# Performance work log

Measured on AMD Instinct MI355X. Metric: run time of the kernel, lower is better.

Reference implementation:

```python
import jax, jax.numpy as jnp
import numpy as np

N_NODES = 100000
N_EDGES = 1600000
IN_DIM = 256
HEADS = 4
OUT_DIM = 32
NEG_SLOPE = 0.2


def setup_inputs() -> dict:
    key = jax.random.key(0)
    ks = jax.random.split(key, 6)
    x = jax.random.normal(ks[0], (N_NODES, IN_DIM), dtype=jnp.float32)
    # xavier-ish init scale for fc and attention vectors
    W = jax.random.normal(ks[1], (IN_DIM, HEADS * OUT_DIM), dtype=jnp.float32) * (1.0 / np.sqrt(IN_DIM))
    attn_l = jax.random.normal(ks[2], (HEADS, OUT_DIM), dtype=jnp.float32) * (1.0 / np.sqrt(OUT_DIM))
    attn_r = jax.random.normal(ks[3], (HEADS, OUT_DIM), dtype=jnp.float32) * (1.0 / np.sqrt(OUT_DIM))
    src = jax.random.randint(ks[4], (N_EDGES,), 0, N_NODES, dtype=jnp.int32)
    dst = jax.random.randint(ks[5], (N_EDGES,), 0, N_NODES, dtype=jnp.int32)
    return {"x": x, "W": W, "attn_l": attn_l, "attn_r": attn_r, "src": src, "dst": dst}


def reference(x, W, attn_l, attn_r, src, dst):
    N = x.shape[0]
    H, D = attn_l.shape
    # shared linear projection (feat_drop = 0)
    feat = (x @ W).reshape(N, H, D)                      # [N,H,D]
    el = jnp.sum(feat * attn_l, axis=-1)                 # [N,H]
    er = jnp.sum(feat * attn_r, axis=-1)                 # [N,H]
    e = jax.nn.leaky_relu(el[src] + er[dst], NEG_SLOPE)  # [E,H]
    # edge softmax over incoming edges of each destination node
    m = jax.ops.segment_max(e, dst, num_segments=N)      # [N,H]
    m = jnp.where(jnp.isfinite(m), m, 0.0)               # zero-in-degree guard
    ex = jnp.exp(e - m[dst])                             # [E,H]
    denom = jax.ops.segment_sum(ex, dst, num_segments=N) # [N,H]
    a = ex / jnp.maximum(denom[dst], 1e-9)               # [E,H] (attn_drop = 0)
    # weighted scatter-add aggregation
    out = jax.ops.segment_sum(a[:, :, None] * feat[src], dst, num_segments=N)  # [N,H,D]
    # head mean (the .mean(1) in GAT1.forward)
    return out.mean(axis=1)                              # [N,D]
```

## Files before the change

kernel.cpp:

```cpp
#include <hip/hip_runtime.h>
#include <math.h>

#define NN 100000
#define NE 1600000
#define IN_DIM 256
#define HD 128
#define NEG_SLOPE 0.2f

#define B1SH 9
#define NPB (1 << B1SH)
#define NB1 ((NN + NPB - 1) / NPB)
#define SC_BLOCKS ((NE / 4 + 1023) / 1024)
#define SCP 392
#define GEMM_BLOCKS ((NN + 63) / 64)
#define D2_GRID (SC_BLOCKS * 5)

typedef __attribute__((ext_vector_type(8))) __bf16 bf16x8;
typedef __attribute__((ext_vector_type(4))) float floatx4;
typedef __attribute__((ext_vector_type(2))) float f32x2;

__device__ inline unsigned short f2bf(float f) {
    unsigned int b = __float_as_uint(f);
    b += 0x7fffu + ((b >> 16) & 1u);
    return (unsigned short)(b >> 16);
}
__device__ inline unsigned int pk(float lo, float hi) {
    return (unsigned int)f2bf(lo) | ((unsigned int)f2bf(hi) << 16);
}
__device__ inline float lrelu(float v) { return (v > 0.f) ? v : v * NEG_SLOPE; }
__device__ inline f32x2 un2(unsigned int v) {
    f32x2 r;
    r.x = __uint_as_float(v << 16);
    r.y = __uint_as_float(v & 0xffff0000u);
    return r;
}

__global__ __launch_bounds__(256) void d1_kernel(const float* __restrict__ W,
                                                 unsigned int* __restrict__ wswz,
                                                 const int4* __restrict__ dst4,
                                                 int* __restrict__ gcnt2dT) {
    __shared__ int cnt[NB1];
    const int t = threadIdx.x;
    if (blockIdx.x < SC_BLOCKS) {
        for (int i = t; i < NB1; i += 256) cnt[i] = 0;
        __syncthreads();
        int base4 = blockIdx.x * 1024;
#pragma unroll
        for (int k = 0; k < 4; ++k) {
            int gi = base4 + k * 256 + t;
            if (gi < NE / 4) {
                int4 d = dst4[gi];
                atomicAdd(&cnt[d.x >> B1SH], 1);
                atomicAdd(&cnt[d.y >> B1SH], 1);
                atomicAdd(&cnt[d.z >> B1SH], 1);
                atomicAdd(&cnt[d.w >> B1SH], 1);
            }
        }
        __syncthreads();
        for (int i = t; i < NB1; i += 256)
            gcnt2dT[i * SCP + blockIdx.x] = cnt[i];
        if (blockIdx.x == 0)
            for (int i = t; i < NB1; i += 256)
                gcnt2dT[i * SCP + SC_BLOCKS] = 0;
    } else {
        int g = (blockIdx.x - SC_BLOCKS) * 256 + t;
        int lane = g & 63;
        int tt = (g >> 6) & 7;
        int c = g >> 9;
        int sub = lane & 15, quad = lane >> 4;
        int n = tt * 16 + sub;
        int kbase = c * 32 + quad * 8;
        unsigned int ob = (unsigned int)g * 4;
#pragma unroll
        for (int i = 0; i < 4; ++i) {
            float lo = W[(size_t)(kbase + 2 * i) * HD + n];
            float hi = W[(size_t)(kbase + 2 * i + 1) * HD + n];
            wswz[ob + i] = pk(lo, hi);
        }
    }
}

__global__ __launch_bounds__(256) void d2_kernel(const float* __restrict__ x,
                                                 const uint4* __restrict__ wswz,
                                                 const float* __restrict__ attn_l,
                                                 const float* __restrict__ attn_r,
                                                 unsigned short* __restrict__ featb,
                                                 float* __restrict__ el,
                                                 float* __restrict__ er,
                                                 const int4* __restrict__ src4,
                                                 const int4* __restrict__ dst4,
                                                 const int* __restrict__ gcnt2dT,
                                                 unsigned int* __restrict__ pkd,
                                                 int* __restrict__ regstart) {
    __shared__ int cnt[NB1];
    __shared__ int gbase[NB1];
    __shared__ int sh[256];
    const int t = threadIdx.x;
    const int bid = blockIdx.x;

    if (bid % 5 == 0) {
        const int b = bid / 5;
        int colsum = 0, mypre = 0;
        if (t < NB1) {
            const int4* rowp = (const int4*)(gcnt2dT + t * SCP);
#pragma unroll 7
            for (int q = 0; q < SCP / 4; ++q) {
                int4 v = rowp[q];
                int s4 = v.x + v.y + v.z + v.w;
                colsum += s4;
                int base = q * 4;
                if (base + 4 <= b) {
                    mypre += s4;
                } else {
                    if (base + 0 < b) mypre += v.x;
                    if (base + 1 < b) mypre += v.y;
                    if (base + 2 < b) mypre += v.z;
                    if (base + 3 < b) mypre += v.w;
                }
            }
        }
        sh[t] = (t < NB1) ? colsum : 0;
        __syncthreads();
        for (int o = 1; o < 256; o <<= 1) {
            int a = (t >= o) ? sh[t - o] : 0;
            __syncthreads();
            sh[t] += a;
            __syncthreads();
        }
        int rstart = sh[t] - ((t < NB1) ? colsum : 0);
        if (t < NB1) gbase[t] = rstart + mypre;
        if (b == 0 && t < NB1) regstart[t] = rstart;
        if (b == 0 && t == 0) regstart[NB1] = NE;
        for (int i = t; i < NB1; i += 256) cnt[i] = 0;
        __syncthreads();

        int base4 = b * 1024;
        unsigned int pkv[16];
        unsigned int brk[16];
#pragma unroll
        for (int k = 0; k < 4; ++k) {
            int gi = base4 + k * 256 + t;
            bool ok = gi < NE / 4;
            int gic = ok ? gi : 0;
            int4 s = src4[gic];
            int4 d = dst4[gic];
            int dd[4] = {d.x, d.y, d.z, d.w};
            int ss[4] = {s.x, s.y, s.z, s.w};
#pragma unroll
            for (int j4 = 0; j4 < 4; ++j4) {
                int e = k * 4 + j4;
                if (ok) {
                    int bk = dd[j4] >> B1SH;
                    int r = atomicAdd(&cnt[bk], 1);
                    brk[e] = ((unsigned int)bk << 12) | (unsigned int)r;
                    pkv[e] = ((unsigned int)(dd[j4] & (NPB - 1)) << 17) | (unsigned int)ss[j4];
                } else {
                    brk[e] = 0xFFFFFFFFu;
                }
            }
        }
        __syncthreads();
#pragma unroll
        for (int e = 0; e < 16; ++e) {
            if (brk[e] != 0xFFFFFFFFu) {
                int bk = brk[e] >> 12;
                int r = brk[e] & 0xFFF;
                pkd[gbase[bk] + r] = pkv[e];
            }
        }
    } else {
        const int gb = bid - 1 - bid / 5;
        if (gb >= GEMM_BLOCKS) return;
        const int lane = t & 63, wv = t >> 6;
        const int sub = lane & 15, quad = lane >> 4;
        const int row0 = gb * 64 + wv * 16;

        int m = row0 + sub;
        if (m >= NN) m = NN - 1;
        const float* xp = x + (size_t)m * IN_DIM + quad * 8;

        bf16x8 af[8];
#pragma unroll
        for (int h = 0; h < 2; ++h) {
            float4 raw[4][2];
#pragma unroll
            for (int c = 0; c < 4; ++c) {
                raw[c][0] = *(const float4*)(xp + (h * 4 + c) * 32);
                raw[c][1] = *(const float4*)(xp + (h * 4 + c) * 32 + 4);
            }
#pragma unroll
            for (int c = 0; c < 4; ++c) {
                uint4 au;
                au.x = pk(raw[c][0].x, raw[c][0].y);
                au.y = pk(raw[c][0].z, raw[c][0].w);
                au.z = pk(raw[c][1].x, raw[c][1].y);
                au.w = pk(raw[c][1].z, raw[c][1].w);
                af[h * 4 + c] = __builtin_bit_cast(bf16x8, au);
            }
        }

        floatx4 acc[8];
#pragma unroll
        for (int tt = 0; tt < 8; ++tt) acc[tt] = (floatx4){0.f, 0.f, 0.f, 0.f};

#pragma unroll
        for (int c = 0; c < 8; ++c) {
            uint4 bu[8];
#pragma unroll
            for (int tt = 0; tt < 8; ++tt) bu[tt] = wswz[(c * 8 + tt) * 64 + lane];
#pragma unroll
            for (int tt = 0; tt < 8; ++tt) {
                bf16x8 bfr = __builtin_bit_cast(bf16x8, bu[tt]);
                acc[tt] = __builtin_amdgcn_mfma_f32_16x16x32_bf16(af[c], bfr, acc[tt], 0, 0, 0);
            }
        }

        float al[8], ar[8];
#pragma unroll
        for (int tt = 0; tt < 8; ++tt) {
            al[tt] = attn_l[tt * 16 + sub];
            ar[tt] = attn_r[tt * 16 + sub];
        }

#pragma unroll
        for (int r = 0; r < 4; ++r) {
            int row = row0 + quad * 4 + r;
            uint4 fv;
            fv.x = pk(acc[0][r], acc[1][r]);
            fv.y = pk(acc[2][r], acc[3][r]);
            fv.z = pk(acc[4][r], acc[5][r]);
            fv.w = pk(acc[6][r], acc[7][r]);
            float pl[4], pr[4];
#pragma unroll
            for (int hh = 0; hh < 4; ++hh) {
                pl[hh] = acc[2 * hh][r] * al[2 * hh] + acc[2 * hh + 1][r] * al[2 * hh + 1];
                pr[hh] = acc[2 * hh][r] * ar[2 * hh] + acc[2 * hh + 1][r] * ar[2 * hh + 1];
            }
#pragma unroll
            for (int o = 1; o < 16; o <<= 1) {
#pragma unroll
                for (int hh = 0; hh < 4; ++hh) {
                    pl[hh] += __shfl_xor(pl[hh], o);
                    pr[hh] += __shfl_xor(pr[hh], o);
                }
            }
            if (row < NN) {
                *(uint4*)(featb + (size_t)row * HD + sub * 8) = fv;
                if (sub < 4) {
                    float vl = (sub == 0) ? pl[0] : (sub == 1) ? pl[1] : (sub == 2) ? pl[2] : pl[3];
                    float vr = (sub == 0) ? pr[0] : (sub == 1) ? pr[1] : (sub == 2) ? pr[2] : pr[3];
                    el[row * 4 + sub] = vl;
                    er[row * 4 + sub] = vr;
                }
            }
        }
    }
}

__global__ __launch_bounds__(1024) void build_kernel(const unsigned int* __restrict__ pkd,
                                                     const int* __restrict__ regstart,
                                                     int* __restrict__ offs,
                                                     int* __restrict__ csr_src) {
    __shared__ int fcnt[NPB];
    __shared__ int foffs[NPB];
    __shared__ int ssc[NPB];
    int b = blockIdx.x, t = threadIdx.x;
    int rs = regstart[b], re = regstart[b + 1];
    int n = re - rs;
    if (b == 0 && t == 0) offs[NN] = NE;

    if (t < NPB) fcnt[t] = 0;
    __syncthreads();
    for (int i = t; i < n; i += 1024) {
        unsigned int v = pkd[rs + i];
        atomicAdd(&fcnt[v >> 17], 1);
    }
    __syncthreads();
    int a = 0;
    if (t < NPB) { a = fcnt[t]; ssc[t] = a; }
    __syncthreads();
    for (int o = 1; o < NPB; o <<= 1) {
        int u = 0;
        if (t < NPB && t >= o) u = ssc[t - o];
        __syncthreads();
        if (t < NPB) ssc[t] += u;
        __syncthreads();
    }
    if (t < NPB) {
        foffs[t] = ssc[t] - a;
        int node = b * NPB + t;
        if (node < NN) offs[node] = rs + foffs[t];
        fcnt[t] = 0;
    }
    __syncthreads();
    int i = t;
    for (; i + 3072 < n; i += 4096) {
        unsigned int v0 = pkd[rs + i];
        unsigned int v1 = pkd[rs + i + 1024];
        unsigned int v2 = pkd[rs + i + 2048];
        unsigned int v3 = pkd[rs + i + 3072];
        int j0 = v0 >> 17, j1 = v1 >> 17, j2 = v2 >> 17, j3 = v3 >> 17;
        int r0 = atomicAdd(&fcnt[j0], 1);
        int r1 = atomicAdd(&fcnt[j1], 1);
        int r2 = atomicAdd(&fcnt[j2], 1);
        int r3 = atomicAdd(&fcnt[j3], 1);
        csr_src[rs + foffs[j0] + r0] = (int)(v0 & 0x1FFFFu);
        csr_src[rs + foffs[j1] + r1] = (int)(v1 & 0x1FFFFu);
        csr_src[rs + foffs[j2] + r2] = (int)(v2 & 0x1FFFFu);
        csr_src[rs + foffs[j3] + r3] = (int)(v3 & 0x1FFFFu);
    }
    for (; i < n; i += 1024) {
        unsigned int v = pkd[rs + i];
        int j = v >> 17;
        int r = atomicAdd(&fcnt[j], 1);
        csr_src[rs + foffs[j] + r] = (int)(v & 0x1FFFFu);
    }
}

#define CH 32
__global__ __launch_bounds__(256, 4) void aggregate_kernel(const uint4* __restrict__ featu4,
                                                           const float4* __restrict__ el4,
                                                           const float4* __restrict__ er4,
                                                           const int* __restrict__ offs,
                                                           const int* __restrict__ csr_src,
                                                           float* __restrict__ out) {
    __shared__ int    s_sv[4][4][CH + 1];
    __shared__ float4 s_a4[4][4][CH + 1];
    __shared__ int sdeg[16], smap[16];

    const int tid = threadIdx.x;
    const int lane = tid & 63, wv = tid >> 6;
    const int g = lane >> 4, sub = lane & 15;

    if (tid < 16) {
        int n0 = blockIdx.x * 16 + tid;
        sdeg[tid] = offs[n0 + 1] - offs[n0];
    }
    __syncthreads();
    if (tid < 16) {
        int d = sdeg[tid];
        int rank = 0;
#pragma unroll
        for (int j = 0; j < 16; ++j) {
            int dj = sdeg[j];
            rank += (dj < d) || (dj == d && j < tid);
        }
        smap[rank] = blockIdx.x * 16 + tid;
    }
    __syncthreads();
    const int node = smap[wv * 4 + g];
    const int beg = offs[node], end = offs[node + 1];

    const float4 erv = er4[node];
    float4 sm = make_float4(0.f, 0.f, 0.f, 0.f);
    f32x2 acc2[4];
#pragma unroll
    for (int i = 0; i < 4; ++i) acc2[i] = (f32x2){0.f, 0.f};

    for (int c0 = beg; c0 < end; c0 += CH) {
        int cnt = end - c0;
        if (cnt > CH) cnt = CH;

        int svr[2];
#pragma unroll
        for (int t = 0; t < 2; ++t) {
            int slot = sub + t * 16;
            int sv = (slot < cnt) ? csr_src[c0 + slot] : 0;
            svr[t] = sv;
            s_sv[wv][g][slot] = sv * 16;
        }

        uint4 ua[8], ub[8];
#pragma unroll
        for (int e = 0; e < 8; ++e)
            ua[e] = featu4[(size_t)s_sv[wv][g][e] + sub];

#pragma unroll
        for (int t = 0; t < 2; ++t) {
            int slot = sub + t * 16;
            float4 w = make_float4(0.f, 0.f, 0.f, 0.f);
            if (slot < cnt) {
                float4 e = el4[svr[t]];
                w.x = __expf(lrelu(e.x + erv.x));
                w.y = __expf(lrelu(e.y + erv.y));
                w.z = __expf(lrelu(e.z + erv.z));
                w.w = __expf(lrelu(e.w + erv.w));
                sm.x += w.x; sm.y += w.y; sm.z += w.z; sm.w += w.w;
            }
            s_a4[wv][g][slot] = w;
        }

        int rounds = (cnt + 7) >> 3;
        int jr = 0;
        while (true) {
            bool m1 = (jr + 1) < rounds;
            if (m1) {
                int nb = (jr + 1) << 3;
#pragma unroll
                for (int e = 0; e < 8; ++e)
                    ub[e] = featu4[(size_t)s_sv[wv][g][nb + e] + sub];
            }
            {
                int jb = jr << 3;
#pragma unroll
                for (int e = 0; e < 8; ++e) {
                    float4 we = s_a4[wv][g][jb + e];
                    uint4 u = ua[e];
                    f32x2 w0 = {we.x, we.x}, w1 = {we.y, we.y};
                    f32x2 w2 = {we.z, we.z}, w3 = {we.w, we.w};
                    acc2[0] = __builtin_elementwise_fma(w0, un2(u.x), acc2[0]);
                    acc2[1] = __builtin_elementwise_fma(w1, un2(u.y), acc2[1]);
                    acc2[2] = __builtin_elementwise_fma(w2, un2(u.z), acc2[2]);
                    acc2[3] = __builtin_elementwise_fma(w3, un2(u.w), acc2[3]);
                }
            }
            ++jr;
            if (!m1) break;
            bool m2 = (jr + 1) < rounds;
            if (m2) {
                int nb = (jr + 1) << 3;
#pragma unroll
                for (int e = 0; e < 8; ++e)
                    ua[e] = featu4[(size_t)s_sv[wv][g][nb + e] + sub];
            }
            {
                int jb = jr << 3;
#pragma unroll
                for (int e = 0; e < 8; ++e) {
                    float4 we = s_a4[wv][g][jb + e];
                    uint4 u = ub[e];
                    f32x2 w0 = {we.x, we.x}, w1 = {we.y, we.y};
                    f32x2 w2 = {we.z, we.z}, w3 = {we.w, we.w};
                    acc2[0] = __builtin_elementwise_fma(w0, un2(u.x), acc2[0]);
                    acc2[1] = __builtin_elementwise_fma(w1, un2(u.y), acc2[1]);
                    acc2[2] = __builtin_elementwise_fma(w2, un2(u.z), acc2[2]);
                    acc2[3] = __builtin_elementwise_fma(w3, un2(u.w), acc2[3]);
                }
            }
            ++jr;
            if (!m2) break;
        }
    }

#pragma unroll
    for (int o = 1; o < 16; o <<= 1) {
        sm.x += __shfl_xor(sm.x, o);
        sm.y += __shfl_xor(sm.y, o);
        sm.z += __shfl_xor(sm.z, o);
        sm.w += __shfl_xor(sm.w, o);
    }
    float ix = 1.f / fmaxf(sm.x, 1e-9f);
    float iy = 1.f / fmaxf(sm.y, 1e-9f);
    float iz = 1.f / fmaxf(sm.z, 1e-9f);
    float iw = 1.f / fmaxf(sm.w, 1e-9f);
    float ox = 0.25f * (acc2[0].x * ix + acc2[1].x * iy + acc2[2].x * iz + acc2[3].x * iw);
    float oy = 0.25f * (acc2[0].y * ix + acc2[1].y * iy + acc2[2].y * iz + acc2[3].y * iw);
    out[node * 32 + sub]      = ox;
    out[node * 32 + 16 + sub] = oy;
}

extern "C" void kernel_launch(void* const* d_in, const int* in_sizes, int n_in,
                              void* d_out, int out_size, void* d_ws, size_t ws_size,
                              hipStream_t stream) {
    const float* x      = (const float*)d_in[0];
    const float* W      = (const float*)d_in[1];
    const float* attn_l = (const float*)d_in[2];
    const float* attn_r = (const float*)d_in[3];
    const int*   src    = (const int*)d_in[4];
    const int*   dst    = (const int*)d_in[5];
    float* out = (float*)d_out;

    char* p = (char*)d_ws;
    auto alloc = [&](size_t bytes) -> void* {
        void* r = (void*)p;
        p += (bytes + 255) & ~(size_t)255;
        return r;
    };
    unsigned short* featb = (unsigned short*)alloc((size_t)NN * HD * 2);
    unsigned int*   wswz  = (unsigned int*)alloc(4096 * 16);
    float* el      = (float*)alloc((size_t)NN * 4 * 4);
    float* er      = (float*)alloc((size_t)NN * 4 * 4);
    int*   offs    = (int*)alloc((size_t)(NN + 1) * 4);
    unsigned int* pkd = (unsigned int*)alloc((size_t)NE * 4);
    int*   csr     = (int*)alloc((size_t)NE * 4);
    int*   gcnt2dT = (int*)alloc((size_t)NB1 * SCP * 4);
    int*   regstart= (int*)alloc((size_t)(NB1 + 1) * 4);

    d1_kernel<<<SC_BLOCKS + 16, 256, 0, stream>>>(W, wswz, (const int4*)dst, gcnt2dT);
    d2_kernel<<<D2_GRID, 256, 0, stream>>>(x, (const uint4*)wswz, attn_l, attn_r,
                                           featb, el, er,
                                           (const int4*)src, (const int4*)dst,
                                           gcnt2dT, pkd, regstart);
    build_kernel<<<NB1, 1024, 0, stream>>>(pkd, regstart, offs, csr);
    aggregate_kernel<<<NN / 16, 256, 0, stream>>>((const uint4*)featb, (const float4*)el,
                                                  (const float4*)er, offs, csr, out);
}
```

Before: 301.5 us.

## Use persistent GEMM blocks with weights staged in LDS

The GEMM part of the fused d2 kernel now runs a fixed set of 512 persistent blocks instead of one block per 64 rows. Each block copies the 64KB swizzled bf16 weight matrix into shared memory once, and each wave loops over 16-row groups, reading B fragments from LDS rather than global memory. The grid is reordered so scatter blocks come first, followed by the GEMM blocks, instead of being interleaved 1:4. The 64KB of LDS per block limits occupancy and may reduce overlap with the scatter work. The row bound check is removed, which is safe because NN is divisible by 16.

```diff
diff --git a/kernel.cpp b/kernel.cpp
--- a/kernel.cpp
+++ b/kernel.cpp
@@ -12,8 +12,9 @@
 #define NB1 ((NN + NPB - 1) / NPB)
 #define SC_BLOCKS ((NE / 4 + 1023) / 1024)
 #define SCP 392
-#define GEMM_BLOCKS ((NN + 63) / 64)
-#define D2_GRID (SC_BLOCKS * 5)
+#define NGB 512
+#define NGROUPS (NN / 16)
+#define D2_GRID (SC_BLOCKS + NGB)
 
 typedef __attribute__((ext_vector_type(8))) __bf16 bf16x8;
 typedef __attribute__((ext_vector_type(4))) float floatx4;
@@ -92,14 +93,15 @@
                                                  const int* __restrict__ gcnt2dT,
                                                  unsigned int* __restrict__ pkd,
                                                  int* __restrict__ regstart) {
-    __shared__ int cnt[NB1];
-    __shared__ int gbase[NB1];
-    __shared__ int sh[256];
+    __shared__ uint4 smem[4096];
     const int t = threadIdx.x;
     const int bid = blockIdx.x;
 
-    if (bid % 5 == 0) {
-        const int b = bid / 5;
+    if (bid < SC_BLOCKS) {
+        int* cnt   = (int*)smem;
+        int* gbase = cnt + NB1;
+        int* sh    = gbase + NB1;
+        const int b = bid;
         int colsum = 0, mypre = 0;
         if (t < NB1) {
             const int4* rowp = (const int4*)(gcnt2dT + t * SCP);
@@ -169,82 +171,78 @@
             }
         }
     } else {
-        const int gb = bid - 1 - bid / 5;
-        if (gb >= GEMM_BLOCKS) return;
+        const int gb = bid - SC_BLOCKS;
+#pragma unroll
+        for (int i = 0; i < 16; ++i)
+            smem[i * 256 + t] = wswz[i * 256 + t];
+        __syncthreads();
+
         const int lane = t & 63, wv = t >> 6;
         const int sub = lane & 15, quad = lane >> 4;
-        const int row0 = gb * 64 + wv * 16;
-
-        int m = row0 + sub;
-        if (m >= NN) m = NN - 1;
-        const float* xp = x + (size_t)m * IN_DIM + quad * 8;
-
-        bf16x8 af[8];
-#pragma unroll
-        for (int h = 0; h < 2; ++h) {
-            float4 raw[4][2];
-#pragma unroll
-            for (int c = 0; c < 4; ++c) {
-                raw[c][0] = *(const float4*)(xp + (h * 4 + c) * 32);
-                raw[c][1] = *(const float4*)(xp + (h * 4 + c) * 32 + 4);
-            }
-#pragma unroll
-            for (int c = 0; c < 4; ++c) {
+
+        float al[8], ar[8];
+#pragma unroll
+        for (int tt = 0; tt < 8; ++tt) {
+            al[tt] = attn_l[tt * 16 + sub];
+            ar[tt] = attn_r[tt * 16 + sub];
+        }
+
+        for (int gg = gb * 4 + wv; gg < NGROUPS; gg += NGB * 4) {
+            const int row0 = gg * 16;
+            const float* xp = x + (size_t)(row0 + sub) * IN_DIM + quad * 8;
+
+            float4 raw[8][2];
+#pragma unroll
+            for (int c = 0; c < 8; ++c) {
+                raw[c][0] = *(const float4*)(xp + c * 32);
+                raw[c][1] = *(const float4*)(xp + c * 32 + 4);
+            }
+            bf16x8 af[8];
+#pragma unroll
+            for (int c = 0; c < 8; ++c) {
                 uint4 au;
                 au.x = pk(raw[c][0].x, raw[c][0].y);
                 au.y = pk(raw[c][0].z, raw[c][0].w);
                 au.z = pk(raw[c][1].x, raw[c][1].y);
                 au.w = pk(raw[c][1].z, raw[c][1].w);
-                af[h * 4 + c] = __builtin_bit_cast(bf16x8, au);
-            }
-        }
-
-        floatx4 acc[8];
-#pragma unroll
-        for (int tt = 0; tt < 8; ++tt) acc[tt] = (floatx4){0.f, 0.f, 0.f, 0.f};
-
-#pragma unroll
-        for (int c = 0; c < 8; ++c) {
-            uint4 bu[8];
-#pragma unroll
-            for (int tt = 0; tt < 8; ++tt) bu[tt] = wswz[(c * 8 + tt) * 64 + lane];
-#pragma unroll
-            for (int tt = 0; tt < 8; ++tt) {
-                bf16x8 bfr = __builtin_bit_cast(bf16x8, bu[tt]);
-                acc[tt] = __builtin_amdgcn_mfma_f32_16x16x32_bf16(af[c], bfr, acc[tt], 0, 0, 0);
-            }
-        }
-
-        float al[8], ar[8];
-#pragma unroll
-        for (int tt = 0; tt < 8; ++tt) {
-            al[tt] = attn_l[tt * 16 + sub];
-            ar[tt] = attn_r[tt * 16 + sub];
-        }
-
-#pragma unroll
-        for (int r = 0; r < 4; ++r) {
-            int row = row0 + quad * 4 + r;
-            uint4 fv;
-            fv.x = pk(acc[0][r], acc[1][r]);
-            fv.y = pk(acc[2][r], acc[3][r]);
-            fv.z = pk(acc[4][r], acc[5][r]);
-            fv.w = pk(acc[6][r], acc[7][r]);
-            float pl[4], pr[4];
-#pragma unroll
-            for (int hh = 0; hh < 4; ++hh) {
-                pl[hh] = acc[2 * hh][r] * al[2 * hh] + acc[2 * hh + 1][r] * al[2 * hh + 1];
-                pr[hh] = acc[2 * hh][r] * ar[2 * hh] + acc[2 * hh + 1][r] * ar[2 * hh + 1];
-            }
-#pragma unroll
-            for (int o = 1; o < 16; o <<= 1) {
+                af[c] = __builtin_bit_cast(bf16x8, au);
+            }
+
+            floatx4 acc[8];
+#pragma unroll
+            for (int tt = 0; tt < 8; ++tt) acc[tt] = (floatx4){0.f, 0.f, 0.f, 0.f};
+
+#pragma unroll
+            for (int c = 0; c < 8; ++c) {
+#pragma unroll
+                for (int tt = 0; tt < 8; ++tt) {
+                    bf16x8 bfr = __builtin_bit_cast(bf16x8, smem[(c * 8 + tt) * 64 + lane]);
+                    acc[tt] = __builtin_amdgcn_mfma_f32_16x16x32_bf16(af[c], bfr, acc[tt], 0, 0, 0);
+                }
+            }
+
+#pragma unroll
+            for (int r = 0; r < 4; ++r) {
+                int row = row0 + quad * 4 + r;
+                uint4 fv;
+                fv.x = pk(acc[0][r], acc[1][r]);
+                fv.y = pk(acc[2][r], acc[3][r]);
+                fv.z = pk(acc[4][r], acc[5][r]);
+                fv.w = pk(acc[6][r], acc[7][r]);
+                float pl[4], pr[4];
 #pragma unroll
                 for (int hh = 0; hh < 4; ++hh) {
-                    pl[hh] += __shfl_xor(pl[hh], o);
-                    pr[hh] += __shfl_xor(pr[hh], o);
-                }
-            }
-            if (row < NN) {
+                    pl[hh] = acc[2 * hh][r] * al[2 * hh] + acc[2 * hh + 1][r] * al[2 * hh + 1];
+                    pr[hh] = acc[2 * hh][r] * ar[2 * hh] + acc[2 * hh + 1][r] * ar[2 * hh + 1];
+                }
+#pragma unroll
+                for (int o = 1; o < 16; o <<= 1) {
+#pragma unroll
+                    for (int hh = 0; hh < 4; ++hh) {
+                        pl[hh] += __shfl_xor(pl[hh], o);
+                        pr[hh] += __shfl_xor(pr[hh], o);
+                    }
+                }
                 *(uint4*)(featb + (size_t)row * HD + sub * 8) = fv;
                 if (sub < 4) {
                     float vl = (sub == 0) ? pl[0] : (sub == 1) ? pl[1] : (sub == 2) ? pl[2] : pl[3];
```

New measurement: 316.7 us. 1.05x slower.
